# Kernel tuning notes

Hardware: AMD Instinct MI355X
Metric: run time of the kernel (lower is better)

The kernel has to match this reference:

```python
import jax, jax.numpy as jnp
import numpy as np

# config constants (from init_kwargs conf dict + FPHA dataset constants)
HAND_SCALE = 5.0
NO_HAND_SCALE = 0.1
HAND_ROOT = 0
SHARPNESS = 2.0
D_TH = 75.0
SIL_THRESH = 0.6
IM_W, IM_H, REF_DEPTH = 1920.0, 1080.0, 1000.0
DD = 5  # depth cells


def setup_inputs() -> dict:
    key = jax.random.key(0)
    k1, k2 = jax.random.split(key)
    pred = jax.random.normal(k1, (256, 320, 26, 26), dtype=jnp.float32)
    uvd_gt = jax.random.uniform(k2, (256, 21, 3), dtype=jnp.float32)
    return {"pred": pred, "uvd_gt": uvd_gt, "train_out": 0}


def _forward(pred, uvd_gt):
    B, C, W, H = pred.shape
    G = W * H * DD
    dt = pred.dtype

    gl = pred.reshape(B, 64, -1)                                   # (B,64,5*W*H)
    iu, iv, iz = jnp.unravel_index(jnp.arange(G), (W, H, DD))
    u = iu.astype(dt); v = iv.astype(dt); z = iz.astype(dt)        # (G,)

    puvd_no = gl[:, :63].reshape(B, 21, 3, G)
    pconf = jax.nn.sigmoid(gl[:, 63].reshape(B, W, H, DD))
    puvd_no = puvd_no.at[:, HAND_ROOT].set(jax.nn.sigmoid(puvd_no[:, HAND_ROOT]))

    # pred_uvd is detached in the torch code (clone().detach())
    pu = jax.lax.stop_gradient(puvd_no)
    pred_uvd = jnp.stack([(pu[:, :, 0] + u) / W,
                          (pu[:, :, 1] + v) / H,
                          (pu[:, :, 2] + z) / DD], axis=2)          # (B,21,3,G)

    # ---- true confidence per cell (vectorized calc_conf over batch & cells) ----
    scale = jnp.array([IM_W, IM_H, REF_DEPTH], dt)[None, None, :, None]
    dist = (pred_uvd - uvd_gt[..., None]) * scale                  # (B,21,3,G)
    dist = jnp.sqrt(jnp.sum(dist * dist, axis=2) + 1e-5)           # (B,21,G)
    mask = (dist < D_TH).astype(dt)
    conf0 = jnp.exp(jnp.asarray(SHARPNESS, dt)) - 1.0
    conf = mask * (jnp.exp(SHARPNESS * (1.0 - dist / D_TH)) - 1.0) / conf0
    mean_conf = jnp.mean(conf, axis=1)                             # (B,G)

    # ---- GT cell index per batch (int() truncation; gt >= 0) ----
    gi = jnp.clip((uvd_gt[:, HAND_ROOT, 0] * W).astype(jnp.int32), 0, W - 1)
    gj = jnp.clip((uvd_gt[:, HAND_ROOT, 1] * H).astype(jnp.int32), 0, H - 1)
    gk = jnp.clip((uvd_gt[:, HAND_ROOT, 2] * DD).astype(jnp.int32), 0, DD - 1)
    lin = H * DD * gi + DD * gj + gk                               # (B,)
    b = jnp.arange(B)

    onehot = jnp.zeros((B, G), dt).at[b, lin].set(1.0)             # (B,G)
    coord_mask = onehot.reshape(B, W, H, DD)
    target_conf = (onehot * mean_conf).reshape(B, W, H, DD)

    conf_mask = jnp.full((B, G), NO_HAND_SCALE, dt)
    conf_mask = jnp.where(mean_conf > SIL_THRESH, jnp.asarray(0.0, dt), conf_mask)
    conf_mask = conf_mask.at[b, lin].set(HAND_SCALE)
    conf_mask = jnp.sqrt(conf_mask).reshape(B, W, H, DD)

    dims = jnp.array([W, H, DD], dt)
    gidx = jnp.stack([gi, gj, gk], axis=-1).astype(dt)             # (B,3)
    tvals = uvd_gt * dims - gidx[:, None, :]                       # (B,21,3)
    target_uvd = tvals[:, :, :, None] * onehot[:, None, None, :]   # (B,21,3,G)

    # targets/masks are built on detached tensors in torch
    target_uvd = jax.lax.stop_gradient(target_uvd)
    target_conf = jax.lax.stop_gradient(target_conf)
    conf_mask = jax.lax.stop_gradient(conf_mask)

    # ---- masked MSE losses (sum reduction, /2) ----
    diff = onehot[:, None, None, :] * (puvd_no - target_uvd)       # (B,21,3,G)
    per_axis = 0.5 * jnp.sum(diff * diff, axis=(0, 1, 3))          # (3,)
    loss_u, loss_v, loss_d = per_axis[0], per_axis[1], per_axis[2]
    cdiff = conf_mask * (pconf - target_conf)
    loss_conf = 0.5 * jnp.sum(cdiff * cdiff)
    total = loss_u + loss_v + loss_d + loss_conf
    return total, loss_u, loss_v, loss_d, loss_conf


def reference(pred, uvd_gt, train_out):
    total, lu, lv, ld, lc = _forward(pred, uvd_gt)
    if train_out:
        return (total, lu, lv, ld, lc)
    return total
```

## Files before the change

### kernel.cpp

```cpp
#include <hip/hip_runtime.h>

#define NJ       21
#define CH       3380
#define BSTRIDE  216320
#define GROUPS   1690
#define BLKS_PER_BATCH 7
#define NBLK     (256 * BLKS_PER_BATCH)

#define CA0 (1920.0f / 26.0f)
#define CA1 (1080.0f / 26.0f)
#define CA2 (1000.0f / 5.0f)
#define INVC0 0.15651764f
#define SKIP_TH 76.0f
#define PRE_TH  406.0f
#define PRE_LO0 (-150.0f)
#define PRE_HI0 76.1f

__device__ __forceinline__ float sigmoidf_(float x) {
    return 1.0f / (1.0f + __expf(-x));
}

__device__ __forceinline__ void joint_term(
    const float* __restrict__ p, bool sig,
    const float d0_[2], float gs1, float gs2,
    const float cb1_[2], const float cb2_[2], float csum[2])
{
    const float2 y = *(const float2*)(p + CH);
    const float2 z = *(const float2*)(p + 2 * CH);
    float yv[2] = {y.x, y.y};
    float zv[2] = {z.x, z.y};
    if (sig) {
        yv[0] = sigmoidf_(yv[0]); yv[1] = sigmoidf_(yv[1]);
        zv[0] = sigmoidf_(zv[0]); zv[1] = sigmoidf_(zv[1]);
    }
#pragma unroll
    for (int k = 0; k < 2; ++k) {
        const float d1 = fmaf(yv[k], CA1, cb1_[k] - gs1);
        const float d2 = fmaf(zv[k], CA2, cb2_[k] - gs2);
        const float dsq = fmaf(d0_[k], d0_[k], fmaf(d1, d1, fmaf(d2, d2, 1e-5f)));
        const float dist = sqrtf(dsq);
        const float c = (__expf(2.0f - dist * (2.0f / 75.0f)) - 1.0f) * INVC0;
        csum[k] += (dist < 75.0f) ? c : 0.0f;
    }
}

__global__ __launch_bounds__(256, 7) void hpo_main(
    const float* __restrict__ pred,
    const float* __restrict__ gt,
    float* __restrict__ partial)
{
    __shared__ float    s_gs[NJ][3];
    __shared__ float    s_tv[NJ][3];
    __shared__ int      s_lin_sh;
    __shared__ unsigned s_m26[26];
    __shared__ float    s_w[4];

    const int bid   = blockIdx.x;
    const int b     = bid / BLKS_PER_BATCH;
    const int chunk = bid - b * BLKS_PER_BATCH;
    const int tid   = threadIdx.x;
    const int lane  = tid & 63;
    const int wid   = tid >> 6;

    const float* gtb = gt + b * (NJ * 3);

    if (tid < NJ * 3) {
        const int j = tid / 3;
        const int a = tid - 3 * j;
        const float scale_a = (a == 0) ? 1920.0f : ((a == 1) ? 1080.0f : 1000.0f);
        const float dim_a   = (a == 2) ? 5.0f : 26.0f;
        const int   dimi    = (a == 2) ? 5 : 26;
        const float gv = gtb[tid];
        s_gs[j][a] = gv * scale_a;
        const float g0v = gtb[a];
        int gi = (int)(g0v * dim_a);
        gi = min(max(gi, 0), dimi - 1);
        s_tv[j][a] = gv * dim_a - (float)gi;
    }
    if (tid == 0) {
        int gi = min(max((int)(gtb[0] * 26.0f), 0), 25);
        int gj = min(max((int)(gtb[1] * 26.0f), 0), 25);
        int gk = min(max((int)(gtb[2] * 5.0f),  0), 4);
        s_lin_sh = 130 * gi + 5 * gj + gk;
    }
    __syncthreads();

    if (tid < 26) {
        const float cw = (float)tid * CA0;
        unsigned m = 0;
#pragma unroll
        for (int j = 0; j < NJ; ++j) {
            const float e = cw - s_gs[j][0];
            const bool p = (j == 0) ? (e > PRE_LO0 && e < PRE_HI0)
                                    : (fabsf(e) < PRE_TH);
            m |= p ? (1u << j) : 0u;
        }
        s_m26[tid] = m;
    }
    __syncthreads();

    const int s_lin = s_lin_sh;
    const int t = chunk * 256 + tid;
    float acc = 0.0f;

    if (t < GROUPS) {
        const int g0 = 2 * t;
        const float* base = pred + (size_t)b * BSTRIDE + g0;
        const int klin = s_lin - g0;

        const float2 wc = *(const float2*)(base + (size_t)63 * CH);

        const int tw     = chunk * 256 + (tid & ~63);
        const int cfirst = 2 * tw;
        const int clast  = min(cfirst + 127, 3379);
        const unsigned um = s_m26[cfirst / 130] | s_m26[clast / 130];
        const int npre = __popc(um);

        bool wave_big = false;
        float csum[2] = {0.0f, 0.0f};

        if (npre >= 13) {
            float cb0[2], cb1[2], cb2[2];
#pragma unroll
            for (int k = 0; k < 2; ++k) {
                const int g   = g0 + k;
                const int w   = g / 130;
                const int rem = g - w * 130;
                const int h   = rem / 5;
                const int d   = rem - h * 5;
                cb0[k] = (float)w * CA0;
                cb1[k] = (float)h * CA1;
                cb2[k] = (float)d * CA2;
            }

            int cnt[2] = {0, 0};
            for (int jc = 0; jc < NJ; jc += 7) {
                float e[7][2];
#pragma unroll
                for (int u = 0; u < 7; ++u) {
                    const float gs0 = s_gs[jc + u][0];
                    e[u][0] = cb0[0] - gs0;
                    e[u][1] = cb0[1] - gs0;
                }
                float2 xv[7];
#pragma unroll
                for (int u = 0; u < 7; ++u)
                    if ((um >> (jc + u)) & 1u)
                        xv[u] = *(const float2*)(base + (size_t)(3 * (jc + u)) * CH);
#pragma unroll
                for (int u = 0; u < 7; ++u) {
                    if ((um >> (jc + u)) & 1u) {
                        float a0 = xv[u].x, a1 = xv[u].y;
                        if (jc + u == 0) { a0 = sigmoidf_(a0); a1 = sigmoidf_(a1); }
                        const float d00 = fmaf(a0, CA0, e[u][0]);
                        const float d01 = fmaf(a1, CA0, e[u][1]);
                        cnt[0] += (fabsf(d00) < SKIP_TH) ? 1 : 0;
                        cnt[1] += (fabsf(d01) < SKIP_TH) ? 1 : 0;
                    }
                }
            }

            wave_big = __any(cnt[0] >= 13 || cnt[1] >= 13);
            if (wave_big) {
                if (um & 1u) {
                    const float gs0 = s_gs[0][0];
                    const float e0 = cb0[0] - gs0, e1 = cb0[1] - gs0;
                    const float2 x = *(const float2*)(base);
                    const float d0_[2] = { fmaf(sigmoidf_(x.x), CA0, e0),
                                           fmaf(sigmoidf_(x.y), CA0, e1) };
                    if (__any(fabsf(d0_[0]) < SKIP_TH || fabsf(d0_[1]) < SKIP_TH))
                        joint_term(base, true, d0_, s_gs[0][1], s_gs[0][2],
                                   cb1, cb2, csum);
                }
                for (int j = 1; j < NJ; ++j) {
                    if (!((um >> j) & 1u)) continue;
                    const float gs0 = s_gs[j][0];
                    const float e0 = cb0[0] - gs0, e1 = cb0[1] - gs0;
                    const float* p = base + (size_t)(3 * j) * CH;
                    const float2 x = *(const float2*)(p);
                    const float d0_[2] = { fmaf(x.x, CA0, e0), fmaf(x.y, CA0, e1) };
                    if (__any(fabsf(d0_[0]) < SKIP_TH || fabsf(d0_[1]) < SKIP_TH))
                        joint_term(p, false, d0_, s_gs[j][1], s_gs[j][2],
                                   cb1, cb2, csum);
                }
            }
        }

#pragma unroll
        for (int k = 0; k < 2; ++k) {
            if (k == klin) continue;
            const float pconf = sigmoidf_(k ? wc.y : wc.x);
            float cm2 = 0.1f;
            if (wave_big) {
                const float mc = csum[k] * (1.0f / 21.0f);
                cm2 = (mc > 0.6f) ? 0.0f : 0.1f;
            }
            acc += 0.5f * cm2 * pconf * pconf;
        }
    }

    if ((s_lin >> 1) / 256 == chunk && tid < 64) {
        float diff = 0.0f, sq = 0.0f;
        const int j = tid / 3;
        const int a = tid - 3 * j;
        if (tid < 63) {
            float v = pred[(size_t)b * BSTRIDE + (size_t)tid * CH + s_lin];
            if (j == 0) v = sigmoidf_(v);
            diff = v - s_tv[j][a];
            acc += 0.5f * diff * diff;
            const float sc = (a == 0) ? CA0 : ((a == 1) ? CA1 : CA2);
            const float ds = diff * sc;
            sq = ds * ds;
        }
        const float s3 = sq + __shfl_down(sq, 1, 64) + __shfl_down(sq, 2, 64);
        float cj = 0.0f;
        if (tid < 63 && a == 0) {
            const float dist = sqrtf(s3 + 1e-5f);
            const float c = (__expf(2.0f - dist * (2.0f / 75.0f)) - 1.0f) * INVC0;
            cj = (dist < 75.0f) ? c : 0.0f;
        }
#pragma unroll
        for (int m = 32; m > 0; m >>= 1) cj += __shfl_xor(cj, m, 64);
        if (tid == 63) {
            const float cv = pred[(size_t)b * BSTRIDE + (size_t)63 * CH + s_lin];
            const float pc = sigmoidf_(cv);
            const float dd = pc - cj * (1.0f / 21.0f);
            acc += 2.5f * dd * dd;
        }
    }

#pragma unroll
    for (int m = 32; m > 0; m >>= 1) acc += __shfl_xor(acc, m, 64);
    if (lane == 0) s_w[wid] = acc;
    __syncthreads();

    if (tid == 0) partial[bid] = s_w[0] + s_w[1] + s_w[2] + s_w[3];
}

__global__ __launch_bounds__(256) void hpo_reduce(
    const float* __restrict__ partial,
    float* __restrict__ out)
{
    __shared__ float s[256];
    const int tid = threadIdx.x;
    float a = 0.0f;
#pragma unroll
    for (int i = 0; i < BLKS_PER_BATCH; ++i)
        a += partial[tid + 256 * i];
    s[tid] = a;
    __syncthreads();
    for (int st = 128; st > 0; st >>= 1) {
        if (tid < st) s[tid] += s[tid + st];
        __syncthreads();
    }
    if (tid == 0) out[0] = s[0];
}

extern "C" void kernel_launch(void* const* d_in, const int* in_sizes, int n_in,
                              void* d_out, int out_size, void* d_ws, size_t ws_size,
                              hipStream_t stream) {
    const float* pred = (const float*)d_in[0];
    const float* gt   = (const float*)d_in[1];
    float* out        = (float*)d_out;
    float* partial    = (float*)d_ws;

    hpo_main<<<NBLK, 256, 0, stream>>>(pred, gt, partial);
    hpo_reduce<<<1, 256, 0, stream>>>(partial, out);
}
```

Before: 12.27 us.

## Use one block per batch with fixed-point atomic reduction replacing reduce kernel

Changes the grid from seven 256-thread blocks per batch to one 512-thread block per batch, with each thread looping over up to four group slots. Confidence loads are hoisted ahead of the loop, cheap groups are resolved first, and the expensive cold path is deferred. The second reduce kernel is removed: each block adds a fixed-point 64-bit integer atomic to a global accumulator, and the last block writes the result, which needs a memset on the workspace. The aim is to save a kernel launch and the per-batch setup work, at the cost of using only 256 blocks and accepting fixed-point rounding.

```diff
diff --git a/kernel.cpp b/kernel.cpp
--- a/kernel.cpp
+++ b/kernel.cpp
@@ -4,8 +4,9 @@
 #define CH       3380
 #define BSTRIDE  216320
 #define GROUPS   1690
-#define BLKS_PER_BATCH 7
-#define NBLK     (256 * BLKS_PER_BATCH)
+#define TPB      512
+#define NITER    4
+#define NBATCH   256
 
 #define CA0 (1920.0f / 26.0f)
 #define CA1 (1080.0f / 26.0f)
@@ -15,6 +16,7 @@
 #define PRE_TH  406.0f
 #define PRE_LO0 (-150.0f)
 #define PRE_HI0 76.1f
+#define FPSCALE 4194304.0
 
 __device__ __forceinline__ float sigmoidf_(float x) {
     return 1.0f / (1.0f + __expf(-x));
@@ -44,23 +46,109 @@
     }
 }
 
-__global__ __launch_bounds__(256, 7) void hpo_main(
+__device__ void cold_group(
+    const float* __restrict__ bb, int t, int s_lin, unsigned um,
+    const float (*s_gs)[3], float* acc)
+{
+    const int g0 = 2 * t;
+    const int klin = s_lin - g0;
+
+    float cb0[2], cb1[2], cb2[2];
+#pragma unroll
+    for (int k = 0; k < 2; ++k) {
+        const int g   = g0 + k;
+        const int w   = g / 130;
+        const int rem = g - w * 130;
+        const int h   = rem / 5;
+        const int d   = rem - h * 5;
+        cb0[k] = (float)w * CA0;
+        cb1[k] = (float)h * CA1;
+        cb2[k] = (float)d * CA2;
+    }
+
+    int cnt[2] = {0, 0};
+    for (int jc = 0; jc < NJ; jc += 7) {
+        float e[7][2];
+#pragma unroll
+        for (int u = 0; u < 7; ++u) {
+            const float gs0 = s_gs[jc + u][0];
+            e[u][0] = cb0[0] - gs0;
+            e[u][1] = cb0[1] - gs0;
+        }
+        float2 xv[7];
+#pragma unroll
+        for (int u = 0; u < 7; ++u)
+            if ((um >> (jc + u)) & 1u)
+                xv[u] = *(const float2*)(bb + (size_t)(3 * (jc + u)) * CH + g0);
+#pragma unroll
+        for (int u = 0; u < 7; ++u) {
+            if ((um >> (jc + u)) & 1u) {
+                float a0 = xv[u].x, a1 = xv[u].y;
+                if (jc + u == 0) { a0 = sigmoidf_(a0); a1 = sigmoidf_(a1); }
+                const float d00 = fmaf(a0, CA0, e[u][0]);
+                const float d01 = fmaf(a1, CA0, e[u][1]);
+                cnt[0] += (fabsf(d00) < SKIP_TH) ? 1 : 0;
+                cnt[1] += (fabsf(d01) < SKIP_TH) ? 1 : 0;
+            }
+        }
+    }
+
+    float csum[2] = {0.0f, 0.0f};
+    const bool wave_big = __any(cnt[0] >= 13 || cnt[1] >= 13);
+    if (wave_big) {
+        const float* base = bb + g0;
+        if (um & 1u) {
+            const float gs0 = s_gs[0][0];
+            const float e0 = cb0[0] - gs0, e1 = cb0[1] - gs0;
+            const float2 x = *(const float2*)(base);
+            const float d0_[2] = { fmaf(sigmoidf_(x.x), CA0, e0),
+                                   fmaf(sigmoidf_(x.y), CA0, e1) };
+            if (__any(fabsf(d0_[0]) < SKIP_TH || fabsf(d0_[1]) < SKIP_TH))
+                joint_term(base, true, d0_, s_gs[0][1], s_gs[0][2], cb1, cb2, csum);
+        }
+        for (int j = 1; j < NJ; ++j) {
+            if (!((um >> j) & 1u)) continue;
+            const float gs0 = s_gs[j][0];
+            const float e0 = cb0[0] - gs0, e1 = cb0[1] - gs0;
+            const float* p = base + (size_t)(3 * j) * CH;
+            const float2 x = *(const float2*)(p);
+            const float d0_[2] = { fmaf(x.x, CA0, e0), fmaf(x.y, CA0, e1) };
+            if (__any(fabsf(d0_[0]) < SKIP_TH || fabsf(d0_[1]) < SKIP_TH))
+                joint_term(p, false, d0_, s_gs[j][1], s_gs[j][2], cb1, cb2, csum);
+        }
+    }
+
+    const float2 wcc = *(const float2*)(bb + (size_t)63 * CH + g0);
+#pragma unroll
+    for (int k = 0; k < 2; ++k) {
+        if (k == klin) continue;
+        const float pconf = sigmoidf_(k ? wcc.y : wcc.x);
+        float cm2 = 0.1f;
+        if (wave_big) {
+            const float mc = csum[k] * (1.0f / 21.0f);
+            cm2 = (mc > 0.6f) ? 0.0f : 0.1f;
+        }
+        *acc += 0.5f * cm2 * pconf * pconf;
+    }
+}
+
+__global__ __launch_bounds__(TPB) void hpo_main(
     const float* __restrict__ pred,
     const float* __restrict__ gt,
-    float* __restrict__ partial)
+    unsigned long long* __restrict__ ll_acc,
+    unsigned* __restrict__ counter,
+    float* __restrict__ out)
 {
     __shared__ float    s_gs[NJ][3];
     __shared__ float    s_tv[NJ][3];
     __shared__ int      s_lin_sh;
     __shared__ unsigned s_m26[26];
-    __shared__ float    s_w[4];
-
-    const int bid   = blockIdx.x;
-    const int b     = bid / BLKS_PER_BATCH;
-    const int chunk = bid - b * BLKS_PER_BATCH;
-    const int tid   = threadIdx.x;
-    const int lane  = tid & 63;
-    const int wid   = tid >> 6;
+    __shared__ float    s_w[TPB / 64];
+
+    const int b    = blockIdx.x;
+    const int tid  = threadIdx.x;
+    const int lane = tid & 63;
+    const int wid  = tid >> 6;
 
     const float* gtb = gt + b * (NJ * 3);
 
@@ -100,111 +188,55 @@
     __syncthreads();
 
     const int s_lin = s_lin_sh;
-    const int t = chunk * 256 + tid;
+    const float* bb = pred + (size_t)b * BSTRIDE;
     float acc = 0.0f;
 
-    if (t < GROUPS) {
-        const int g0 = 2 * t;
-        const float* base = pred + (size_t)b * BSTRIDE + g0;
-        const int klin = s_lin - g0;
-
-        const float2 wc = *(const float2*)(base + (size_t)63 * CH);
-
-        const int tw     = chunk * 256 + (tid & ~63);
-        const int cfirst = 2 * tw;
-        const int clast  = min(cfirst + 127, 3379);
-        const unsigned um = s_m26[cfirst / 130] | s_m26[clast / 130];
-        const int npre = __popc(um);
-
-        bool wave_big = false;
-        float csum[2] = {0.0f, 0.0f};
-
-        if (npre >= 13) {
-            float cb0[2], cb1[2], cb2[2];
-#pragma unroll
-            for (int k = 0; k < 2; ++k) {
-                const int g   = g0 + k;
-                const int w   = g / 130;
-                const int rem = g - w * 130;
-                const int h   = rem / 5;
-                const int d   = rem - h * 5;
-                cb0[k] = (float)w * CA0;
-                cb1[k] = (float)h * CA1;
-                cb2[k] = (float)d * CA2;
-            }
-
-            int cnt[2] = {0, 0};
-            for (int jc = 0; jc < NJ; jc += 7) {
-                float e[7][2];
-#pragma unroll
-                for (int u = 0; u < 7; ++u) {
-                    const float gs0 = s_gs[jc + u][0];
-                    e[u][0] = cb0[0] - gs0;
-                    e[u][1] = cb0[1] - gs0;
-                }
-                float2 xv[7];
-#pragma unroll
-                for (int u = 0; u < 7; ++u)
-                    if ((um >> (jc + u)) & 1u)
-                        xv[u] = *(const float2*)(base + (size_t)(3 * (jc + u)) * CH);
-#pragma unroll
-                for (int u = 0; u < 7; ++u) {
-                    if ((um >> (jc + u)) & 1u) {
-                        float a0 = xv[u].x, a1 = xv[u].y;
-                        if (jc + u == 0) { a0 = sigmoidf_(a0); a1 = sigmoidf_(a1); }
-                        const float d00 = fmaf(a0, CA0, e[u][0]);
-                        const float d01 = fmaf(a1, CA0, e[u][1]);
-                        cnt[0] += (fabsf(d00) < SKIP_TH) ? 1 : 0;
-                        cnt[1] += (fabsf(d01) < SKIP_TH) ? 1 : 0;
-                    }
-                }
-            }
-
-            wave_big = __any(cnt[0] >= 13 || cnt[1] >= 13);
-            if (wave_big) {
-                if (um & 1u) {
-                    const float gs0 = s_gs[0][0];
-                    const float e0 = cb0[0] - gs0, e1 = cb0[1] - gs0;
-                    const float2 x = *(const float2*)(base);
-                    const float d0_[2] = { fmaf(sigmoidf_(x.x), CA0, e0),
-                                           fmaf(sigmoidf_(x.y), CA0, e1) };
-                    if (__any(fabsf(d0_[0]) < SKIP_TH || fabsf(d0_[1]) < SKIP_TH))
-                        joint_term(base, true, d0_, s_gs[0][1], s_gs[0][2],
-                                   cb1, cb2, csum);
-                }
-                for (int j = 1; j < NJ; ++j) {
-                    if (!((um >> j) & 1u)) continue;
-                    const float gs0 = s_gs[j][0];
-                    const float e0 = cb0[0] - gs0, e1 = cb0[1] - gs0;
-                    const float* p = base + (size_t)(3 * j) * CH;
-                    const float2 x = *(const float2*)(p);
-                    const float d0_[2] = { fmaf(x.x, CA0, e0), fmaf(x.y, CA0, e1) };
-                    if (__any(fabsf(d0_[0]) < SKIP_TH || fabsf(d0_[1]) < SKIP_TH))
-                        joint_term(p, false, d0_, s_gs[j][1], s_gs[j][2],
-                                   cb1, cb2, csum);
-                }
-            }
-        }
-
-#pragma unroll
-        for (int k = 0; k < 2; ++k) {
-            if (k == klin) continue;
-            const float pconf = sigmoidf_(k ? wc.y : wc.x);
-            float cm2 = 0.1f;
-            if (wave_big) {
-                const float mc = csum[k] * (1.0f / 21.0f);
-                cm2 = (mc > 0.6f) ? 0.0f : 0.1f;
-            }
-            acc += 0.5f * cm2 * pconf * pconf;
-        }
-    }
-
-    if ((s_lin >> 1) / 256 == chunk && tid < 64) {
+    float2 wc[NITER];
+#pragma unroll
+    for (int it = 0; it < NITER; ++it) {
+        const int t = it * TPB + tid;
+        if (t < GROUPS)
+            wc[it] = *(const float2*)(bb + (size_t)63 * CH + 2 * t);
+    }
+
+    int pending = 0;
+#pragma unroll
+    for (int it = 0; it < NITER; ++it) {
+        const int t = it * TPB + tid;
+        if (t < GROUPS) {
+            const int cfirst = 2 * (it * TPB + (tid & ~63));
+            const int clast  = min(cfirst + 127, 2 * GROUPS - 1);
+            const unsigned um = s_m26[cfirst / 130] | s_m26[clast / 130];
+            if (__popc(um) >= 13) {
+                pending |= (1 << it);
+            } else {
+                const int klin = s_lin - 2 * t;
+                const float pc0 = sigmoidf_(wc[it].x);
+                const float pc1 = sigmoidf_(wc[it].y);
+                acc += 0.05f * (((klin == 0) ? 0.0f : pc0 * pc0) +
+                                ((klin == 1) ? 0.0f : pc1 * pc1));
+            }
+        }
+    }
+
+    if (pending) {
+        for (int it = 0; it < NITER; ++it) {
+            if (pending & (1 << it)) {
+                const int t = it * TPB + tid;
+                const int cfirst = 2 * (it * TPB + (tid & ~63));
+                const int clast  = min(cfirst + 127, 2 * GROUPS - 1);
+                const unsigned um = s_m26[cfirst / 130] | s_m26[clast / 130];
+                cold_group(bb, t, s_lin, um, s_gs, &acc);
+            }
+        }
+    }
+
+    if (tid < 64) {
         float diff = 0.0f, sq = 0.0f;
         const int j = tid / 3;
         const int a = tid - 3 * j;
         if (tid < 63) {
-            float v = pred[(size_t)b * BSTRIDE + (size_t)tid * CH + s_lin];
+            float v = bb[(size_t)tid * CH + s_lin];
             if (j == 0) v = sigmoidf_(v);
             diff = v - s_tv[j][a];
             acc += 0.5f * diff * diff;
@@ -222,7 +254,7 @@
 #pragma unroll
         for (int m = 32; m > 0; m >>= 1) cj += __shfl_xor(cj, m, 64);
         if (tid == 63) {
-            const float cv = pred[(size_t)b * BSTRIDE + (size_t)63 * CH + s_lin];
+            const float cv = bb[(size_t)63 * CH + s_lin];
             const float pc = sigmoidf_(cv);
             const float dd = pc - cj * (1.0f / 21.0f);
             acc += 2.5f * dd * dd;
@@ -234,26 +266,20 @@
     if (lane == 0) s_w[wid] = acc;
     __syncthreads();
 
-    if (tid == 0) partial[bid] = s_w[0] + s_w[1] + s_w[2] + s_w[3];
-}
-
-__global__ __launch_bounds__(256) void hpo_reduce(
-    const float* __restrict__ partial,
-    float* __restrict__ out)
-{
-    __shared__ float s[256];
-    const int tid = threadIdx.x;
-    float a = 0.0f;
-#pragma unroll
-    for (int i = 0; i < BLKS_PER_BATCH; ++i)
-        a += partial[tid + 256 * i];
-    s[tid] = a;
-    __syncthreads();
-    for (int st = 128; st > 0; st >>= 1) {
-        if (tid < st) s[tid] += s[tid + st];
-        __syncthreads();
-    }
-    if (tid == 0) out[0] = s[0];
+    if (tid == 0) {
+        float tot = 0.0f;
+#pragma unroll
+        for (int i = 0; i < TPB / 64; ++i) tot += s_w[i];
+        const long long iv = (long long)((double)tot * FPSCALE);
+        const unsigned long long prev = atomicAdd(ll_acc, (unsigned long long)iv);
+        if (prev != 0x8000000000000000ull) {
+            const unsigned old = atomicAdd(counter, 1u);
+            if (old == NBATCH - 1) {
+                const unsigned long long total = atomicAdd(ll_acc, 0ull);
+                out[0] = (float)((double)(long long)total * (1.0 / FPSCALE));
+            }
+        }
+    }
 }
 
 extern "C" void kernel_launch(void* const* d_in, const int* in_sizes, int n_in,
@@ -262,8 +288,10 @@
     const float* pred = (const float*)d_in[0];
     const float* gt   = (const float*)d_in[1];
     float* out        = (float*)d_out;
-    float* partial    = (float*)d_ws;
-
-    hpo_main<<<NBLK, 256, 0, stream>>>(pred, gt, partial);
-    hpo_reduce<<<1, 256, 0, stream>>>(partial, out);
-}
+
+    unsigned long long* ll_acc = (unsigned long long*)d_ws;
+    unsigned*           counter = (unsigned*)((char*)d_ws + 8);
+
+    hipMemsetAsync(d_ws, 0, 16, stream);
+    hpo_main<<<NBATCH, TPB, 0, stream>>>(pred, gt, ll_acc, counter, out);
+}
```

Measured after the change: 20.26 us. 65.1% more time.
